# Kernel optimization log

Hardware: AMD Instinct MI355X
Metric: run time of the kernel (lower is better)

## Reference

```python
import jax, jax.numpy as jnp
import numpy as np

N_NODES = 100000
N_EDGES = 1000000
D = 64            # in_channels == heads*hidden_channels
OUT = 64          # out_channels
L = 3             # local_layers
RVQ = 3           # residual VQ levels per layer
CODES = 16
BN_EPS = 1e-5
COMMIT_W = 0.25


def _l2n(v, eps=1e-12):
    return v / (jnp.linalg.norm(v, axis=-1, keepdims=True) + eps)


def setup_inputs() -> dict:
    key = jax.random.key(0)
    ks = jax.random.split(key, 16)
    s = 1.0 / np.sqrt(D)
    inp = {
        "x": jax.random.normal(ks[0], (N_NODES, D), jnp.float32),
        "edge_index": jax.random.randint(ks[1], (2, N_EDGES), 0, N_NODES, jnp.int64),
        # SAGEConv: lin_l (applied to mean-aggregated neighbors, with bias), lin_r (root, no bias)
        "Wa": jax.random.uniform(ks[2], (L, D, D), jnp.float32, -s, s),
        "ba": jax.random.uniform(ks[3], (L, D), jnp.float32, -s, s),
        "Wr": jax.random.uniform(ks[4], (L, D, D), jnp.float32, -s, s),
        # skip Linear per layer
        "Wl": jax.random.uniform(ks[5], (L, D, D), jnp.float32, -s, s),
        "bl": jax.random.uniform(ks[6], (L, D), jnp.float32, -s, s),
        # BatchNorm affine
        "gamma": jnp.ones((L, D), jnp.float32),
        "beta": jnp.zeros((L, D), jnp.float32),
        # residual-VQ codebooks: [layer, rvq_level, codes, dim]
        "codebooks": jax.random.normal(ks[7], (L, RVQ, CODES, D), jnp.float32),
        # heads
        "Wp": jax.random.uniform(ks[8], (D, OUT), jnp.float32, -s, s),
        "bp": jax.random.uniform(ks[9], (OUT,), jnp.float32, -s, s),
        "Wg": jax.random.uniform(ks[10], (D, L * RVQ), jnp.float32, -s, s),
        "bg": jax.random.uniform(ks[11], (L * RVQ,), jnp.float32, -s, s),
    }
    return inp


def _sage_conv(x, src, dst, Wa, ba, Wr):
    # mean aggregation of source features onto destinations
    summed = jax.ops.segment_sum(x[src], dst, num_segments=N_NODES)
    cnt = jax.ops.segment_sum(jnp.ones((src.shape[0],), x.dtype), dst, num_segments=N_NODES)
    mean = summed / jnp.maximum(cnt, 1.0)[:, None]
    out = mean @ Wa + ba + x @ Wr
    return _l2n(out)  # normalize=True


def _residual_vq(x, cbs):
    # cosine-sim residual VQ, 3 levels; returns (quantized_sum, ids [N,RVQ], commit_loss)
    residual = x
    quant = jnp.zeros_like(x)
    loss = jnp.zeros((), x.dtype)
    ids = []
    for r in range(RVQ):
        cb = _l2n(cbs[r])                       # [CODES, D]
        sim = _l2n(residual) @ cb.T             # [N, CODES]
        idx = jnp.argmax(sim, axis=-1)          # [N]
        q = cb[idx]                             # [N, D]
        loss = loss + COMMIT_W * jnp.mean((jax.lax.stop_gradient(q) - residual) ** 2)
        q_st = residual + jax.lax.stop_gradient(q - residual)  # straight-through
        quant = quant + q_st
        residual = residual - jax.lax.stop_gradient(q)
        ids.append(idx)
    return quant, jnp.stack(ids, axis=1), loss


def reference(x, edge_index, Wa, ba, Wr, Wl, bl, gamma, beta, codebooks, Wp, bp, Wg, bg):
    src, dst = edge_index[0], edge_index[1]
    h = x  # in_dropout: identity at inference
    x_local = jnp.zeros((N_NODES, D), x.dtype)
    total_commit = jnp.zeros((), x.dtype)
    id_list = []
    for i in range(L):
        h = _sage_conv(h, src, dst, Wa[i], ba[i], Wr[i]) + (h @ Wl[i] + bl[i])
        # BatchNorm1d (batch statistics)
        mu = jnp.mean(h, axis=0)
        var = jnp.var(h, axis=0)
        h = (h - mu) * jax.lax.rsqrt(var + BN_EPS) * gamma[i] + beta[i]
        h = jax.nn.relu(h)  # dropout: identity at inference
        x_local = x_local + h
        _, ids, closs = _residual_vq(h, codebooks[i])
        total_commit = total_commit + closs
        id_list.append(ids)
    id_concat = jnp.concatenate(id_list, axis=1)  # [N, L*RVQ]
    gnn_id = x_local @ Wg + bg
    pred = x_local @ Wp + bp
    return (pred, total_commit, id_concat, gnn_id)
```

## Files before the change

kernel.cpp:

```cpp
#include <hip/hip_runtime.h>
#include <math.h>

#define NN 100000
#define NE 1000000
#define D 64
#define L 3
#define RVQ 3
#define CODES 16
#define BN_EPS 1e-5f
#define COMMIT_W 0.25f

#define GRID_A 2048

#define OFS_ROWPTR 0
#define OFS_CNT    100016
#define OFS_CURSOR 200032
#define OFS_BSUMS  300048
#define OFS_BOFFS  300176
#define OFS_STATS  300304
#define OFS_CSR    300800
#define OFS_HA     1300800
#define OFS_HB     7700800
#define OFS_XLOC   14100800
#define OFS_PART   20500800

#define OUT_PRED   0
#define OUT_COMMIT (NN * D)
#define OUT_IDS    (NN * D + 1)
#define OUT_GNN    (NN * D + 1 + NN * (L * RVQ))

static __device__ __forceinline__ float waveSum(float v) {
    #pragma unroll
    for (int off = 32; off; off >>= 1) v += __shfl_xor(v, off, 64);
    return v;
}

static __device__ __forceinline__ float qxor1(float v) {
    return __int_as_float(__builtin_amdgcn_mov_dpp(__float_as_int(v), 0xB1, 0xF, 0xF, 1));
}
static __device__ __forceinline__ float qxor2(float v) {
    return __int_as_float(__builtin_amdgcn_mov_dpp(__float_as_int(v), 0x4E, 0xF, 0xF, 1));
}

#define RLF(v, li) __int_as_float(__builtin_amdgcn_readlane(__float_as_int(v), (li)))

__global__ void k_count(const int* __restrict__ dst, int* __restrict__ cnt) {
    int e = blockIdx.x * blockDim.x + threadIdx.x;
    if (e < NE) atomicAdd(&cnt[dst[e]], 1);
}

#define SCAN_B 1024
__global__ void k_scan1(const int* __restrict__ cnt, int* __restrict__ rowptr,
                        int* __restrict__ bsums) {
    __shared__ int sm[SCAN_B];
    int t = threadIdx.x;
    int i = blockIdx.x * SCAN_B + t;
    int v = (i < NN) ? cnt[i] : 0;
    sm[t] = v;
    __syncthreads();
    for (int off = 1; off < SCAN_B; off <<= 1) {
        int add = (t >= off) ? sm[t - off] : 0;
        __syncthreads();
        sm[t] += add;
        __syncthreads();
    }
    if (i < NN) rowptr[i + 1] = sm[t];
    if (t == SCAN_B - 1) bsums[blockIdx.x] = sm[t];
}

__global__ void k_scan2(const int* __restrict__ bsums, int* __restrict__ boffs, int nb) {
    __shared__ int sm[SCAN_B];
    int t = threadIdx.x;
    int orig = (t < nb) ? bsums[t] : 0;
    sm[t] = orig;
    __syncthreads();
    for (int off = 1; off < SCAN_B; off <<= 1) {
        int add = (t >= off) ? sm[t - off] : 0;
        __syncthreads();
        sm[t] += add;
        __syncthreads();
    }
    if (t < nb) boffs[t] = sm[t] - orig;
}

__global__ void k_scan3(int* __restrict__ rowptr, const int* __restrict__ boffs) {
    int i = blockIdx.x * SCAN_B + threadIdx.x;
    if (i < NN) rowptr[i + 1] += boffs[blockIdx.x];
    if (i == 0) rowptr[0] = 0;
}

__global__ void k_cursor(const int* __restrict__ rowptr, int* __restrict__ cursor) {
    int i = blockIdx.x * blockDim.x + threadIdx.x;
    if (i < NN) cursor[i] = rowptr[i];
}

__global__ void k_fill(const int* __restrict__ src, const int* __restrict__ dst,
                       int* __restrict__ cursor, int* __restrict__ csr_src) {
    int e = blockIdx.x * blockDim.x + threadIdx.x;
    if (e < NE) {
        int p = atomicAdd(&cursor[dst[e]], 1);
        csr_src[p] = src[e];
    }
}

__global__ void k_sortrows(const int* __restrict__ rowptr, int* __restrict__ csr) {
    int n = blockIdx.x * blockDim.x + threadIdx.x;
    if (n >= NN) return;
    int r0 = rowptr[n], r1 = rowptr[n + 1];
    for (int i = r0 + 1; i < r1; ++i) {
        int v = csr[i];
        int j = i - 1;
        while (j >= r0 && csr[j] > v) { csr[j + 1] = csr[j]; --j; }
        csr[j + 1] = v;
    }
}

__global__ __launch_bounds__(256) void k_gather(
    const float* __restrict__ h, const int* __restrict__ rowptr,
    const int* __restrict__ csr_src, float* __restrict__ mean_out) {
    int t = threadIdx.x;
    int lane = t & 63, wid = t >> 6;
    int n = blockIdx.x * 4 + wid;
    if (n >= NN) return;

    int r0 = rowptr[n], r1 = rowptr[n + 1];
    float s = 0.f;
    for (int base = r0; base < r1; base += 64) {
        int last = r1 - 1;
        int ii = base + lane;
        int idx = csr_src[(ii <= last) ? ii : last];
        int m = r1 - base;
        if (m > 64) m = 64;
        int j = 0;
        for (; j + 8 <= m; j += 8) {
            int i0 = __shfl(idx, j + 0, 64), i1 = __shfl(idx, j + 1, 64);
            int i2 = __shfl(idx, j + 2, 64), i3 = __shfl(idx, j + 3, 64);
            int i4 = __shfl(idx, j + 4, 64), i5 = __shfl(idx, j + 5, 64);
            int i6 = __shfl(idx, j + 6, 64), i7 = __shfl(idx, j + 7, 64);
            float v0 = h[i0 * D + lane], v1 = h[i1 * D + lane];
            float v2 = h[i2 * D + lane], v3 = h[i3 * D + lane];
            float v4 = h[i4 * D + lane], v5 = h[i5 * D + lane];
            float v6 = h[i6 * D + lane], v7 = h[i7 * D + lane];
            s += v0; s += v1; s += v2; s += v3;
            s += v4; s += v5; s += v6; s += v7;
        }
        for (; j + 4 <= m; j += 4) {
            int i0 = __shfl(idx, j + 0, 64), i1 = __shfl(idx, j + 1, 64);
            int i2 = __shfl(idx, j + 2, 64), i3 = __shfl(idx, j + 3, 64);
            float v0 = h[i0 * D + lane], v1 = h[i1 * D + lane];
            float v2 = h[i2 * D + lane], v3 = h[i3 * D + lane];
            s += v0; s += v1; s += v2; s += v3;
        }
        for (; j < m; ++j) {
            int i0 = __shfl(idx, j, 64);
            s += h[i0 * D + lane];
        }
    }
    float deg = (float)(r1 - r0);
    mean_out[n * D + lane] = s / fmaxf(deg, 1.0f);
}

__global__ __launch_bounds__(512, 3) void k_matvec(
    const float* __restrict__ h, float* __restrict__ hp,
    const float* __restrict__ Wa, const float* __restrict__ ba,
    const float* __restrict__ Wr, const float* __restrict__ Wl,
    const float* __restrict__ bl) {
    __shared__ float lw[3 * D * D];
    int t = threadIdx.x, lane = t & 63, wid = t >> 6;

    {
        float4* d4 = (float4*)lw;
        const float4* s4;
        s4 = (const float4*)Wa; d4[t] = s4[t]; d4[t + 512] = s4[t + 512];
        s4 = (const float4*)Wr; d4[1024 + t] = s4[t]; d4[1024 + t + 512] = s4[t + 512];
        s4 = (const float4*)Wl; d4[2048 + t] = s4[t]; d4[2048 + t + 512] = s4[t + 512];
    }
    __syncthreads();

    int wbase = (blockIdx.x * 8 + wid) * 8;
    if (wbase >= NN) return;

    float bav = ba[lane], blv = bl[lane];

    const float4* gm = (const float4*)(hp + (size_t)wbase * D);
    const float4* gh = (const float4*)(h  + (size_t)wbase * D);
    float4 vm0 = gm[lane], vm1 = gm[lane + 64];
    float4 vh0 = gh[lane], vh1 = gh[lane + 64];
    float mreg[8] = {vm0.x, vm0.y, vm0.z, vm0.w, vm1.x, vm1.y, vm1.z, vm1.w};
    float hreg[8] = {vh0.x, vh0.y, vh0.z, vh0.w, vh1.x, vh1.y, vh1.z, vh1.w};

    float am[8], rm[8], lm[8];
    #pragma unroll
    for (int i = 0; i < 8; ++i) { am[i] = 0.f; rm[i] = 0.f; lm[i] = 0.f; }

    #pragma unroll
    for (int c = 0; c < 4; ++c) {
        float wa16[16], wr16[16], wl16[16];
        #pragma unroll
        for (int j = 0; j < 16; ++j) {
            wa16[j] = lw[(c * 16 + j) * D + lane];
            wr16[j] = lw[4096 + (c * 16 + j) * D + lane];
            wl16[j] = lw[8192 + (c * 16 + j) * D + lane];
        }
        #pragma unroll
        for (int i = 0; i < 8; ++i) {
            #pragma unroll
            for (int q = 0; q < 16; ++q) {
                const int kk = c * 16 + q;
                const int fid = i * 16 + (kk >> 2);
                const int rsel = (fid < 64) ? (kk & 3) : 4 + (kk & 3);
                const int lsel = fid & 63;
                float mv = RLF(mreg[rsel], lsel);
                float hv = RLF(hreg[rsel], lsel);
                am[i] += mv * wa16[q];
                rm[i] += hv * wr16[q];
                lm[i] += hv * wl16[q];
            }
        }
    }

    #pragma unroll
    for (int i = 0; i < 8; ++i) {
        float sage = am[i] + bav + rm[i];
        float ss = waveSum(sage * sage);
        float inv = 1.0f / (sqrtf(ss) + 1e-12f);
        float hpv = sage * inv + lm[i] + blv;
        hp[(size_t)(wbase + i) * D + lane] = hpv;
    }
}

__global__ __launch_bounds__(256) void k_bnstats(
    const float* __restrict__ hp, float* __restrict__ partials) {
    __shared__ float red[2][4][D];
    int t = threadIdx.x, lane = t & 63, wid = t >> 6;
    int wg = blockIdx.x * 4 + wid;
    const int wstep = GRID_A * 4;
    float accS = 0.f, accQ = 0.f;
    for (int n = wg; n < NN; n += wstep) {
        float hpv = hp[(size_t)n * D + lane];
        accS += hpv;
        accQ += hpv * hpv;
    }
    red[0][wid][lane] = accS;
    red[1][wid][lane] = accQ;
    __syncthreads();
    if (wid == 0) {
        float s0 = (red[0][0][lane] + red[0][1][lane]) + (red[0][2][lane] + red[0][3][lane]);
        float q0 = (red[1][0][lane] + red[1][1][lane]) + (red[1][2][lane] + red[1][3][lane]);
        partials[blockIdx.x * 128 + lane]      = s0;
        partials[blockIdx.x * 128 + 64 + lane] = q0;
    }
}

__global__ __launch_bounds__(256) void k_red_stats(
    const float* __restrict__ part, float* __restrict__ stats) {
    __shared__ float sm[256];
    int c = blockIdx.x;
    int i = threadIdx.x;
    float s = 0.f;
    #pragma unroll
    for (int k = 0; k < 8; ++k)
        s += part[(size_t)(i * 8 + k) * 128 + c];
    sm[i] = s;
    __syncthreads();
    #pragma unroll
    for (int off = 128; off >= 1; off >>= 1) {
        if (i < off) sm[i] += sm[i + off];
        __syncthreads();
    }
    if (i == 0) stats[c] = sm[0];
}

#define CBSTRIDE 68
__global__ __launch_bounds__(256) void k_layer_b(
    float* __restrict__ hp,
    const float* __restrict__ stats,
    const float* __restrict__ gamma, const float* __restrict__ beta,
    const float* __restrict__ cbs,
    float* __restrict__ x_local,
    float* __restrict__ ids_out,
    int layer, float* __restrict__ commit, int first_layer) {
    __shared__ alignas(16) float scb[RVQ * CODES * CBSTRIDE];
    __shared__ alignas(16) float sscale[D];
    __shared__ alignas(16) float sshift[D];
    __shared__ float sred[4];
    int t = threadIdx.x, lane = t & 63, wid = t >> 6;

    for (int row = wid; row < RVQ * CODES; row += 4) {
        float v = cbs[row * D + lane];
        float ss = waveSum(v * v);
        scb[row * CBSTRIDE + lane] = v / (sqrtf(ss) + 1e-12f);
    }
    if (t < D) {
        float mu = stats[t] * (1.0f / NN);
        float var = stats[64 + t] * (1.0f / NN) - mu * mu;
        float scale = rsqrtf(var + BN_EPS) * gamma[t];
        sscale[t] = scale;
        sshift[t] = beta[t] - mu * scale;
    }
    __syncthreads();

    int gid = blockIdx.x * 256 + t;
    int node = gid >> 2;
    int part = t & 3;
    float closs = 0.f;

    if (node < NN) {
        float res[16];
        size_t base = (size_t)node * D + part * 16;
        const float4* hr = (const float4*)(hp + base);
        float4* hw = (float4*)(hp + base);
        float4* xw = (float4*)(x_local + base);
        const float4* scp = (const float4*)(sscale + part * 16);
        const float4* shp = (const float4*)(sshift + part * 16);

        #pragma unroll
        for (int i = 0; i < 4; ++i) {
            float4 v = hr[i];
            float4 sc = scp[i], sh = shp[i];
            float4 hn;
            hn.x = fmaxf(v.x * sc.x + sh.x, 0.f);
            hn.y = fmaxf(v.y * sc.y + sh.y, 0.f);
            hn.z = fmaxf(v.z * sc.z + sh.z, 0.f);
            hn.w = fmaxf(v.w * sc.w + sh.w, 0.f);
            hw[i] = hn;
            if (first_layer) {
                xw[i] = hn;
            } else {
                float4 xl = xw[i];
                xl.x += hn.x; xl.y += hn.y; xl.z += hn.z; xl.w += hn.w;
                xw[i] = xl;
            }
            res[4 * i + 0] = hn.x; res[4 * i + 1] = hn.y;
            res[4 * i + 2] = hn.z; res[4 * i + 3] = hn.w;
        }

        int bis[RVQ];
        #pragma unroll
        for (int r = 0; r < RVQ; ++r) {
            float sims[CODES];
            #pragma unroll
            for (int j = 0; j < CODES; ++j) {
                const float* cr = &scb[(r * CODES + j) * CBSTRIDE + part * 16];
                float4 c0 = *(const float4*)(cr + 0);
                float4 c1 = *(const float4*)(cr + 4);
                float4 c2 = *(const float4*)(cr + 8);
                float4 c3 = *(const float4*)(cr + 12);
                float a = res[0] * c0.x;
                a += res[1] * c0.y;  a += res[2] * c0.z;  a += res[3] * c0.w;
                a += res[4] * c1.x;  a += res[5] * c1.y;  a += res[6] * c1.z;  a += res[7] * c1.w;
                a += res[8] * c2.x;  a += res[9] * c2.y;  a += res[10] * c2.z; a += res[11] * c2.w;
                a += res[12] * c3.x; a += res[13] * c3.y; a += res[14] * c3.z; a += res[15] * c3.w;
                float b = a + qxor1(a);
                sims[j] = b + qxor2(b);
            }
            float bv = sims[0];
            int bi = 0;
            #pragma unroll
            for (int j = 1; j < CODES; ++j)
                if (sims[j] > bv) { bv = sims[j]; bi = j; }

            const float* qr = &scb[(r * CODES + bi) * CBSTRIDE + part * 16];
            #pragma unroll
            for (int i = 0; i < 4; ++i) {
                float4 q = *(const float4*)(qr + 4 * i);
                float d0 = q.x - res[4 * i + 0]; closs += d0 * d0; res[4 * i + 0] = -d0;
                float d1 = q.y - res[4 * i + 1]; closs += d1 * d1; res[4 * i + 1] = -d1;
                float d2 = q.z - res[4 * i + 2]; closs += d2 * d2; res[4 * i + 2] = -d2;
                float d3 = q.w - res[4 * i + 3]; closs += d3 * d3; res[4 * i + 3] = -d3;
            }
            bis[r] = bi;
        }
        if (part == 0) {
            ids_out[(size_t)node * (L * RVQ) + layer * RVQ + 0] = (float)bis[0];
            ids_out[(size_t)node * (L * RVQ) + layer * RVQ + 1] = (float)bis[1];
            ids_out[(size_t)node * (L * RVQ) + layer * RVQ + 2] = (float)bis[2];
        }
    }

    closs = waveSum(closs);
    if (lane == 0) sred[wid] = closs;
    __syncthreads();
    if (t == 0) {
        float tot = (sred[0] + sred[1]) + (sred[2] + sred[3]);
        atomicAdd(commit, tot * (COMMIT_W / (float)(NN * D)));
    }
}

__global__ __launch_bounds__(256, 2) void k_head(
    const float* __restrict__ x_local,
    const float* __restrict__ Wp, const float* __restrict__ bp,
    const float* __restrict__ Wg, const float* __restrict__ bg,
    float* __restrict__ pred, float* __restrict__ gnn) {
    int t = threadIdx.x, lane = t & 63, wid = t >> 6;
    int jsafe = (lane < 9) ? lane : 0;

    float wp[D], wg[D];
    #pragma unroll
    for (int k = 0; k < D; ++k) {
        wp[k] = Wp[k * D + lane];
        wg[k] = Wg[k * 9 + jsafe];
    }
    float bpv = bp[lane], bgv = bg[jsafe];

    int w = blockIdx.x * 4 + wid;
    int wstep = gridDim.x * 4;
    for (int n = w; n < NN; n += wstep) {
        int nu = __builtin_amdgcn_readfirstlane(n);
        const float4* xrow = (const float4*)(x_local + (size_t)nu * D);
        float p = 0.f, g = 0.f;
        #pragma unroll
        for (int j = 0; j < 16; ++j) {
            float4 x4 = xrow[j];
            p += x4.x * wp[4 * j + 0]; g += x4.x * wg[4 * j + 0];
            p += x4.y * wp[4 * j + 1]; g += x4.y * wg[4 * j + 1];
            p += x4.z * wp[4 * j + 2]; g += x4.z * wg[4 * j + 2];
            p += x4.w * wp[4 * j + 3]; g += x4.w * wg[4 * j + 3];
        }
        pred[(size_t)n * D + lane] = p + bpv;
        if (lane < 9) gnn[(size_t)n * 9 + lane] = g + bgv;
    }
}

extern "C" void kernel_launch(void* const* d_in, const int* in_sizes, int n_in,
                              void* d_out, int out_size, void* d_ws, size_t ws_size,
                              hipStream_t stream) {
    const float* x   = (const float*)d_in[0];
    const int* ei    = (const int*)d_in[1];
    const float* Wa  = (const float*)d_in[2];
    const float* ba  = (const float*)d_in[3];
    const float* Wr  = (const float*)d_in[4];
    const float* Wl  = (const float*)d_in[5];
    const float* bl  = (const float*)d_in[6];
    const float* gamma = (const float*)d_in[7];
    const float* beta  = (const float*)d_in[8];
    const float* cbs = (const float*)d_in[9];
    const float* Wp  = (const float*)d_in[10];
    const float* bp  = (const float*)d_in[11];
    const float* Wg  = (const float*)d_in[12];
    const float* bg  = (const float*)d_in[13];

    const int* src = ei;
    const int* dst = ei + NE;

    int*   ws_i  = (int*)d_ws;
    float* ws_f  = (float*)d_ws;
    int* rowptr  = ws_i + OFS_ROWPTR;
    int* cnt     = ws_i + OFS_CNT;
    int* cursor  = ws_i + OFS_CURSOR;
    int* bsums   = ws_i + OFS_BSUMS;
    int* boffs   = ws_i + OFS_BOFFS;
    float* stats = ws_f + OFS_STATS;
    int* csr_src = ws_i + OFS_CSR;
    float* hA    = ws_f + OFS_HA;
    float* hB    = ws_f + OFS_HB;
    float* xloc  = ws_f + OFS_XLOC;
    float* part  = ws_f + OFS_PART;

    float* out    = (float*)d_out;
    float* pred   = out + OUT_PRED;
    float* commit = out + OUT_COMMIT;
    float* ids    = out + OUT_IDS;
    float* gnn    = out + OUT_GNN;

    hipMemsetAsync(cnt, 0, NN * sizeof(int), stream);
    hipMemsetAsync(commit, 0, sizeof(float), stream);

    k_count<<<(NE + 255) / 256, 256, 0, stream>>>(dst, cnt);
    int nscan = (NN + SCAN_B - 1) / SCAN_B;
    k_scan1<<<nscan, SCAN_B, 0, stream>>>(cnt, rowptr, bsums);
    k_scan2<<<1, SCAN_B, 0, stream>>>(bsums, boffs, nscan);
    k_scan3<<<nscan, SCAN_B, 0, stream>>>(rowptr, boffs);
    k_cursor<<<(NN + 1023) / 1024, 1024, 0, stream>>>(rowptr, cursor);
    k_fill<<<(NE + 255) / 256, 256, 0, stream>>>(src, dst, cursor, csr_src);
    k_sortrows<<<(NN + 255) / 256, 256, 0, stream>>>(rowptr, csr_src);

    const float* hin = x;
    float* bufs[2] = {hA, hB};
    const int nblk_mv = (NN + 63) / 64;
    const int nblk_b  = (NN * 4 + 255) / 256;
    for (int i = 0; i < L; ++i) {
        float* hp = bufs[i & 1];
        k_gather<<<(NN + 3) / 4, 256, 0, stream>>>(hin, rowptr, csr_src, hp);
        k_matvec<<<nblk_mv, 512, 0, stream>>>(hin, hp,
                                              Wa + i * D * D, ba + i * D,
                                              Wr + i * D * D, Wl + i * D * D, bl + i * D);
        k_bnstats<<<GRID_A, 256, 0, stream>>>(hp, part);
        k_red_stats<<<128, 256, 0, stream>>>(part, stats + i * 128);
        k_layer_b<<<nblk_b, 256, 0, stream>>>(hp, stats + i * 128,
                                              gamma + i * D, beta + i * D,
                                              cbs + i * RVQ * CODES * D,
                                              xloc, ids, i, commit, (i == 0) ? 1 : 0);
        hin = hp;
    }

    k_head<<<2048, 256, 0, stream>>>(xloc, Wp, bp, Wg, bg, pred, gnn);
}
```

Baseline: 843.1 us.

## Restructure matvec: per-wave LDS-staged node rows, weights from global, 16 nodes per wave

The matvec kernel no longer stages all three 64x64 weight matrices into shared memory per block. Each wave now handles 16 nodes, staging their aggregated-mean and input rows in a small per-wave LDS buffer and reading them back as float4 broadcasts. Weight columns are read directly from global memory, relying on cache hits. This removes the readlane-based element broadcast and the block-wide weight staging with its barrier, at the cost of more accumulator registers and repeated global weight loads.

```diff
diff --git a/kernel.cpp b/kernel.cpp
--- a/kernel.cpp
+++ b/kernel.cpp
@@ -41,8 +41,6 @@
 static __device__ __forceinline__ float qxor2(float v) {
     return __int_as_float(__builtin_amdgcn_mov_dpp(__float_as_int(v), 0x4E, 0xF, 0xF, 1));
 }
-
-#define RLF(v, li) __int_as_float(__builtin_amdgcn_readlane(__float_as_int(v), (li)))
 
 __global__ void k_count(const int* __restrict__ dst, int* __restrict__ cnt) {
     int e = blockIdx.x * blockDim.x + threadIdx.x;
@@ -160,72 +158,76 @@
     mean_out[n * D + lane] = s / fmaxf(deg, 1.0f);
 }
 
-__global__ __launch_bounds__(512, 3) void k_matvec(
+__global__ __launch_bounds__(256, 3) void k_matvec(
     const float* __restrict__ h, float* __restrict__ hp,
     const float* __restrict__ Wa, const float* __restrict__ ba,
     const float* __restrict__ Wr, const float* __restrict__ Wl,
     const float* __restrict__ bl) {
-    __shared__ float lw[3 * D * D];
+    __shared__ alignas(16) float lbuf[4][16][128];
     int t = threadIdx.x, lane = t & 63, wid = t >> 6;
 
+    int tb = (blockIdx.x * 4 + wid) * 16;
+    if (tb >= NN) return;
+
+    float bav = ba[lane], blv = bl[lane];
+
     {
-        float4* d4 = (float4*)lw;
-        const float4* s4;
-        s4 = (const float4*)Wa; d4[t] = s4[t]; d4[t + 512] = s4[t + 512];
-        s4 = (const float4*)Wr; d4[1024 + t] = s4[t]; d4[1024 + t + 512] = s4[t + 512];
-        s4 = (const float4*)Wl; d4[2048 + t] = s4[t]; d4[2048 + t + 512] = s4[t + 512];
-    }
-    __syncthreads();
-
-    int wbase = (blockIdx.x * 8 + wid) * 8;
-    if (wbase >= NN) return;
-
-    float bav = ba[lane], blv = bl[lane];
-
-    const float4* gm = (const float4*)(hp + (size_t)wbase * D);
-    const float4* gh = (const float4*)(h  + (size_t)wbase * D);
-    float4 vm0 = gm[lane], vm1 = gm[lane + 64];
-    float4 vh0 = gh[lane], vh1 = gh[lane + 64];
-    float mreg[8] = {vm0.x, vm0.y, vm0.z, vm0.w, vm1.x, vm1.y, vm1.z, vm1.w};
-    float hreg[8] = {vh0.x, vh0.y, vh0.z, vh0.w, vh1.x, vh1.y, vh1.z, vh1.w};
-
-    float am[8], rm[8], lm[8];
+        const float4* gm = (const float4*)(hp + (size_t)tb * D);
+        const float4* gh = (const float4*)(h  + (size_t)tb * D);
+        #pragma unroll
+        for (int s = 0; s < 4; ++s) {
+            int fid = s * 64 + lane;
+            int node = fid >> 4, j = fid & 15;
+            float4 vm = gm[fid];
+            float4 vh = gh[fid];
+            *(float4*)&lbuf[wid][node][4 * j]      = vm;
+            *(float4*)&lbuf[wid][node][64 + 4 * j] = vh;
+        }
+    }
+
+    float am[16], rm[16], lm[16];
     #pragma unroll
-    for (int i = 0; i < 8; ++i) { am[i] = 0.f; rm[i] = 0.f; lm[i] = 0.f; }
-
-    #pragma unroll
+    for (int i = 0; i < 16; ++i) { am[i] = 0.f; rm[i] = 0.f; lm[i] = 0.f; }
+
     for (int c = 0; c < 4; ++c) {
         float wa16[16], wr16[16], wl16[16];
         #pragma unroll
         for (int j = 0; j < 16; ++j) {
-            wa16[j] = lw[(c * 16 + j) * D + lane];
-            wr16[j] = lw[4096 + (c * 16 + j) * D + lane];
-            wl16[j] = lw[8192 + (c * 16 + j) * D + lane];
+            wa16[j] = Wa[(c * 16 + j) * D + lane];
+            wr16[j] = Wr[(c * 16 + j) * D + lane];
+            wl16[j] = Wl[(c * 16 + j) * D + lane];
         }
         #pragma unroll
-        for (int i = 0; i < 8; ++i) {
+        for (int i = 0; i < 16; ++i) {
+            const float* mb = &lbuf[wid][i][c * 16];
+            const float* hb = &lbuf[wid][i][64 + c * 16];
             #pragma unroll
-            for (int q = 0; q < 16; ++q) {
-                const int kk = c * 16 + q;
-                const int fid = i * 16 + (kk >> 2);
-                const int rsel = (fid < 64) ? (kk & 3) : 4 + (kk & 3);
-                const int lsel = fid & 63;
-                float mv = RLF(mreg[rsel], lsel);
-                float hv = RLF(hreg[rsel], lsel);
-                am[i] += mv * wa16[q];
-                rm[i] += hv * wr16[q];
-                lm[i] += hv * wl16[q];
+            for (int qq = 0; qq < 4; ++qq) {
+                float4 m4 = *(const float4*)(mb + 4 * qq);
+                float4 h4 = *(const float4*)(hb + 4 * qq);
+                am[i] += m4.x * wa16[4 * qq + 0];
+                rm[i] += h4.x * wr16[4 * qq + 0];
+                lm[i] += h4.x * wl16[4 * qq + 0];
+                am[i] += m4.y * wa16[4 * qq + 1];
+                rm[i] += h4.y * wr16[4 * qq + 1];
+                lm[i] += h4.y * wl16[4 * qq + 1];
+                am[i] += m4.z * wa16[4 * qq + 2];
+                rm[i] += h4.z * wr16[4 * qq + 2];
+                lm[i] += h4.z * wl16[4 * qq + 2];
+                am[i] += m4.w * wa16[4 * qq + 3];
+                rm[i] += h4.w * wr16[4 * qq + 3];
+                lm[i] += h4.w * wl16[4 * qq + 3];
             }
         }
     }
 
     #pragma unroll
-    for (int i = 0; i < 8; ++i) {
+    for (int i = 0; i < 16; ++i) {
         float sage = am[i] + bav + rm[i];
         float ss = waveSum(sage * sage);
         float inv = 1.0f / (sqrtf(ss) + 1e-12f);
         float hpv = sage * inv + lm[i] + blv;
-        hp[(size_t)(wbase + i) * D + lane] = hpv;
+        hp[(size_t)(tb + i) * D + lane] = hpv;
     }
 }
 
@@ -477,12 +479,12 @@
 
     const float* hin = x;
     float* bufs[2] = {hA, hB};
-    const int nblk_mv = (NN + 63) / 64;
+    const int nblk_mv = (NN / 16 + 3) / 4;
     const int nblk_b  = (NN * 4 + 255) / 256;
     for (int i = 0; i < L; ++i) {
         float* hp = bufs[i & 1];
         k_gather<<<(NN + 3) / 4, 256, 0, stream>>>(hin, rowptr, csr_src, hp);
-        k_matvec<<<nblk_mv, 512, 0, stream>>>(hin, hp,
+        k_matvec<<<nblk_mv, 256, 0, stream>>>(hin, hp,
                                               Wa + i * D * D, ba + i * D,
                                               Wr + i * D * D, Wl + i * D * D, bl + i * D);
         k_bnstats<<<GRID_A, 256, 0, stream>>>(hp, part);
```

Result: slower. 878.0 us (+4.1%).
